# Kernel tuning notes

Hardware: AMD Instinct MI355X
Metric: run time of the kernel (lower is better)

Reference implementation:

```python
import jax, jax.numpy as jnp
import numpy as np

NUM_CODES = 1024
CODE_DIM = 256
BETA = 0.25  # commitment cost
N_TOKENS = 131072


def setup_inputs() -> dict:
    key = jax.random.key(0)
    k_z, k_cb = jax.random.split(key)
    z = jax.random.normal(k_z, (N_TOKENS, CODE_DIM), dtype=jnp.float32)
    # nn.init.uniform_(codebook.weight, -1/num_codes, 1/num_codes)
    codebook = jax.random.uniform(
        k_cb, (NUM_CODES, CODE_DIM), dtype=jnp.float32,
        minval=-1.0 / NUM_CODES, maxval=1.0 / NUM_CODES)
    return {"z": z, "codebook": codebook}


def reference(z, codebook):
    # Squared-euclidean distances: ||z||^2 + ||c||^2 - 2 z c^T  -> [N, K]
    d = (jnp.sum(z * z, axis=1, keepdims=True)
         + jnp.sum(codebook * codebook, axis=1)
         - 2.0 * jnp.einsum('nd,kd->nk', z, codebook))
    indices = jnp.argmin(d, axis=1)          # [N] int
    z_q = codebook[indices]                   # gather [N, D]

    sg = jax.lax.stop_gradient
    commit_loss = BETA * jnp.mean((sg(z) - z_q) ** 2)
    codebook_loss = jnp.mean((z - sg(z_q)) ** 2)
    loss = commit_loss + codebook_loss

    z_st = z + sg(z_q - z)                    # straight-through
    return z_st, indices, loss
```

## Files before the change

### kernel.cpp

```cpp
#include <hip/hip_runtime.h>

#define N_TOK 131072
#define KC    1024
#define DIM   256
#define GAP_THR 4e-4f
#define NBLK  (N_TOK / 128)

typedef __attribute__((ext_vector_type(8)))  short bf16x8;
typedef __attribute__((ext_vector_type(16))) float f32x16;

__device__ __forceinline__ unsigned short f2bf(float f) {
    unsigned int u = __float_as_uint(f);
    unsigned int r = (u + 0x7fffu + ((u >> 16) & 1u)) >> 16;
    return (unsigned short)r;
}

#define WS_NEED 7352384ull

__global__ void vq_prep_cb(const float* __restrict__ cb, unsigned short* __restrict__ cb16,
                           float* __restrict__ cnorm, float* __restrict__ cbT,
                           unsigned int* __restrict__ fcounts) {
    if (blockIdx.x == 0 && threadIdx.x < 2) fcounts[threadIdx.x] = 0u;
    int code = blockIdx.x * 4 + (threadIdx.x >> 6);
    int lane = threadIdx.x & 63;
    float4 v = ((const float4*)cb)[(size_t)code * 64 + lane];
    ((float4*)cbT)[(size_t)lane * KC + code] = v;
    ushort4 h;
    h.x = f2bf(v.x); h.y = f2bf(v.y); h.z = f2bf(v.z); h.w = f2bf(v.w);
    ((ushort4*)cb16)[(size_t)code * 64 + lane] = h;
    double s = 0.0;
    s = fma((double)v.x, (double)v.x, s);
    s = fma((double)v.y, (double)v.y, s);
    s = fma((double)v.z, (double)v.z, s);
    s = fma((double)v.w, (double)v.w, s);
    #pragma unroll
    for (int off = 32; off > 0; off >>= 1) s += __shfl_xor(s, off);
    if (lane == 0) cnorm[code] = (float)s;
}

__global__ __launch_bounds__(256)
void vq_scores_fused(const float* __restrict__ z, const unsigned short* __restrict__ cb16,
                     const float* __restrict__ cb, const float* __restrict__ cnorm,
                     float* __restrict__ out, float* __restrict__ out_idx,
                     int* __restrict__ flist, unsigned int* __restrict__ fcount,
                     double* __restrict__ lparts)
{
    __shared__ uint4  cA[128 * 32];
    __shared__ float  cnsL[KC];
    __shared__ float  bm1L[8][128];
    __shared__ float  gm1[128], gm2[128];
    __shared__ int    gid[128];
    __shared__ double sredD[4];

    const int tid = threadIdx.x;
    const int lane = tid & 63;
    const int l31 = lane & 31;
    const int hi  = lane >> 5;
    const int wid = tid >> 6;
    const int wcode = wid >> 1;
    const int wtok  = wid & 1;
    const int tb = blockIdx.x;

    #pragma unroll
    for (int k = 0; k < 4; ++k) cnsL[tid + k * 256] = cnorm[tid + k * 256];
    if (tid < 128) { gm1[tid] = 3.0e38f; gm2[tid] = 3.0e38f; gid[tid] = 0x7fffffff; }

    bf16x8 bfr[2][4][4];
    float zzr[2];
    #pragma unroll
    for (int f = 0; f < 2; ++f) {
        const int t = tb * 128 + wtok * 64 + f * 32 + l31;
        const float* zr = z + (size_t)t * DIM;
        double s = 0.0;
        #pragma unroll
        for (int kb = 0; kb < 4; ++kb)
            #pragma unroll
            for (int ks = 0; ks < 4; ++ks) {
                const int d0 = kb * 64 + ks * 16 + hi * 8;
                float4 x = *(const float4*)(zr + d0);
                float4 y = *(const float4*)(zr + d0 + 4);
                s = fma((double)x.x, (double)x.x, s);
                s = fma((double)x.y, (double)x.y, s);
                s = fma((double)x.z, (double)x.z, s);
                s = fma((double)x.w, (double)x.w, s);
                s = fma((double)y.x, (double)y.x, s);
                s = fma((double)y.y, (double)y.y, s);
                s = fma((double)y.z, (double)y.z, s);
                s = fma((double)y.w, (double)y.w, s);
                bf16x8 v;
                v[0] = (short)f2bf(x.x); v[1] = (short)f2bf(x.y);
                v[2] = (short)f2bf(x.z); v[3] = (short)f2bf(x.w);
                v[4] = (short)f2bf(y.x); v[5] = (short)f2bf(y.y);
                v[6] = (short)f2bf(y.z); v[7] = (short)f2bf(y.w);
                bfr[f][kb][ks] = v;
            }
        s += __shfl_xor(s, 32);
        zzr[f] = (float)s;
    }

    #pragma unroll 1
    for (int cbk = 0; cbk < 8; ++cbk) {
        __syncthreads();
        #pragma unroll
        for (int i = 0; i < 16; ++i) {
            int g = tid + i * 256;
            int c = g >> 5, u = g & 31;
            cA[c * 32 + (u ^ (c & 7))] = ((const uint4*)cb16)[(size_t)(cbk * 128 + c) * 32 + u];
        }
        __syncthreads();

        f32x16 acc[2][2];
        #pragma unroll
        for (int a = 0; a < 2; ++a)
            #pragma unroll
            for (int b = 0; b < 2; ++b)
                #pragma unroll
                for (int r = 0; r < 16; ++r) acc[a][b][r] = 0.0f;

        #pragma unroll
        for (int kb = 0; kb < 4; ++kb)
            #pragma unroll
            for (int ks = 0; ks < 4; ++ks) {
                bf16x8 af[2];
                #pragma unroll
                for (int a = 0; a < 2; ++a) {
                    int c = wcode * 64 + a * 32 + l31;
                    af[a] = ((const bf16x8*)cA)[c * 32 + ((kb * 8 + ks * 2 + hi) ^ (c & 7))];
                }
                #pragma unroll
                for (int a = 0; a < 2; ++a)
                    #pragma unroll
                    for (int b = 0; b < 2; ++b)
                        acc[a][b] = __builtin_amdgcn_mfma_f32_32x32x16_bf16(af[a], bfr[b][kb][ks], acc[a][b], 0, 0, 0);
            }

        float* sm1 = (float*)cA;
        float* sm2 = sm1 + 256;
        int*   sid = (int*)(sm2 + 256);
        #pragma unroll
        for (int tf = 0; tf < 2; ++tf) {
            float c1 = 3.0e38f, c2 = 3.0e38f;
            #pragma unroll
            for (int cf = 0; cf < 2; ++cf)
                #pragma unroll
                for (int r = 0; r < 16; ++r) {
                    int cl = wcode * 64 + cf * 32 + (r & 3) + 8 * (r >> 2) + 4 * hi;
                    float A  = zzr[tf] + cnsL[cbk * 128 + cl];
                    float dq = fmaf(acc[cf][tf][r], -2.0f, A);
                    acc[cf][tf][r] = dq;
                    float hv = fmaxf(c1, dq);
                    c1 = fminf(c1, dq);
                    c2 = fminf(c2, hv);
                }
            int ci = 0x7fffffff;
            #pragma unroll
            for (int cf = 0; cf < 2; ++cf)
                #pragma unroll
                for (int r = 0; r < 16; ++r) {
                    int code = cbk * 128 + wcode * 64 + cf * 32 + (r & 3) + 8 * (r >> 2) + 4 * hi;
                    ci = min(ci, (acc[cf][tf][r] == c1) ? code : 0x7fffffff);
                }
            float o1 = __shfl_xor(c1, 32);
            float o2 = __shfl_xor(c2, 32);
            int  oi = __shfl_xor(ci, 32);
            float nm2 = fminf(fminf(c2, o2), fmaxf(c1, o1));
            int  ni = (o1 < c1 || (o1 == c1 && oi < ci)) ? oi : ci;
            float nm1 = fminf(c1, o1);
            if (hi == 0) {
                int lt = wtok * 64 + tf * 32 + l31;
                sm1[wcode * 128 + lt] = nm1;
                sm2[wcode * 128 + lt] = nm2;
                sid[wcode * 128 + lt] = ni;
            }
        }
        __syncthreads();
        if (tid < 128) {
            float a1 = sm1[tid],       a2 = sm2[tid];       int ai = sid[tid];
            float b1 = sm1[128 + tid], b2 = sm2[128 + tid]; int bi = sid[128 + tid];
            float m1, m2; int ix;
            if (b1 < a1 || (b1 == a1 && bi < ai)) { m1 = b1; ix = bi; m2 = fminf(b2, a1); }
            else                                   { m1 = a1; ix = ai; m2 = fminf(a2, b1); }
            bm1L[cbk][tid] = m1;
            float g1 = gm1[tid], g2 = gm2[tid]; int gi = gid[tid];
            float ng2 = fminf(fminf(g2, m2), fmaxf(g1, m1));
            if (m1 < g1 || (m1 == g1 && ix < gi)) { g1 = m1; gi = ix; }
            gm1[tid] = g1; gm2[tid] = ng2; gid[tid] = gi;
        }
    }
    __syncthreads();

    if (tid < 128) {
        int row = tb * 128 + tid;
        out_idx[row] = (float)gid[tid];
        float g1 = gm1[tid];
        float gap = gm2[tid] - g1;
        int mask = 0;
        #pragma unroll
        for (int c = 0; c < 8; ++c) mask |= (bm1L[c][tid] <= g1 + GAP_THR) ? (1 << c) : 0;
        if (!(gap > GAP_THR)) {
            unsigned int p = atomicAdd(fcount, 1u);
            flist[p] = row | (mask << 17);
        }
    }
    __syncthreads();

    double ls = 0.0;
    const float4* z4  = (const float4*)z;
    const float4* cb4 = (const float4*)cb;
    float4* out4 = (float4*)out;
    #pragma unroll 4
    for (int it = 0; it < 32; ++it) {
        int fi = tid + it * 256;
        int row = fi >> 6, c4 = fi & 63;
        float4 zv = z4[(size_t)(tb * 128 + row) * 64 + c4];
        int idx = gid[row];
        float4 cv = cb4[(size_t)idx * 64 + c4];
        float4 o;
        o.x = zv.x + (cv.x - zv.x);
        o.y = zv.y + (cv.y - zv.y);
        o.z = zv.z + (cv.z - zv.z);
        o.w = zv.w + (cv.w - zv.w);
        out4[(size_t)(tb * 128 + row) * 64 + c4] = o;
        float dx = zv.x - cv.x, dy = zv.y - cv.y, dz = zv.z - cv.z, dw = zv.w - cv.w;
        ls += (double)dx * dx + (double)dy * dy + (double)dz * dz + (double)dw * dw;
    }
    #pragma unroll
    for (int off = 32; off > 0; off >>= 1) ls += __shfl_down(ls, off);
    if (lane == 0) sredD[wid] = ls;
    __syncthreads();
    if (tid == 0) lparts[tb] = (sredD[0] + sredD[1]) + (sredD[2] + sredD[3]);
}

__global__ void vq_expand(const int* __restrict__ flist, const unsigned int* __restrict__ fcount,
                          int* __restrict__ flist2, unsigned int* __restrict__ fcount2,
                          unsigned long long* __restrict__ rck)
{
    const unsigned int cnt = *fcount;
    for (unsigned int i = blockIdx.x * 256 + threadIdx.x; i < cnt; i += gridDim.x * 256) {
        int e = flist[i];
        int row  = e & 0x1FFFF;
        int mask = ((unsigned int)e) >> 17;
        rck[row] = ~0ull;
        while (mask) {
            int c = __ffs(mask) - 1;
            mask &= mask - 1;
            unsigned int p = atomicAdd(fcount2, 1u);
            flist2[p] = row | (c << 17);
        }
    }
}

__global__ __launch_bounds__(256)
void vq_recheck_pairs(const float* __restrict__ z, const float* __restrict__ cbT,
                      const float* __restrict__ cnorm, const int* __restrict__ flist2,
                      const unsigned int* __restrict__ fcount2,
                      unsigned long long* __restrict__ rck)
{
    const int tid  = threadIdx.x;
    const int wid  = tid >> 6;
    const int lane = tid & 63;
    const unsigned int cnt = *fcount2;

    for (unsigned int p = blockIdx.x * 4 + wid; p < cnt; p += gridDim.x * 4) {
        const int e   = flist2[p];
        const int row = e & 0x1FFFF;
        const int blk = ((unsigned int)e) >> 17;
        const float* zr = z + (size_t)row * DIM;

        float4 zv = ((const float4*)zr)[lane];
        double s = 0.0;
        s = fma((double)zv.x, (double)zv.x, s);
        s = fma((double)zv.y, (double)zv.y, s);
        s = fma((double)zv.z, (double)zv.z, s);
        s = fma((double)zv.w, (double)zv.w, s);
        #pragma unroll
        for (int off = 32; off > 0; off >>= 1) s += __shfl_xor(s, off);
        const float zz = (float)s;

        const int c0 = blk * 128 + lane;
        float e0 = 0.0f, e1 = 0.0f;
        #pragma unroll 8
        for (int d4 = 0; d4 < 64; ++d4) {
            float4 zq = ((const float4*)zr)[d4];
            float4 a  = ((const float4*)cbT)[d4 * KC + c0];
            float4 b  = ((const float4*)cbT)[d4 * KC + c0 + 64];
            e0 = fmaf(zq.x, a.x, e0); e0 = fmaf(zq.y, a.y, e0);
            e0 = fmaf(zq.z, a.z, e0); e0 = fmaf(zq.w, a.w, e0);
            e1 = fmaf(zq.x, b.x, e1); e1 = fmaf(zq.y, b.y, e1);
            e1 = fmaf(zq.z, b.z, e1); e1 = fmaf(zq.w, b.w, e1);
        }
        const float dq0 = fmaf(e0, -2.0f, zz + cnorm[c0]);
        const float dq1 = fmaf(e1, -2.0f, zz + cnorm[c0 + 64]);
        unsigned long long k0 = ((unsigned long long)__float_as_uint(dq0) << 32) | (unsigned int)c0;
        unsigned long long k1 = ((unsigned long long)__float_as_uint(dq1) << 32) | (unsigned int)(c0 + 64);
        unsigned long long k = k0 < k1 ? k0 : k1;
        #pragma unroll
        for (int off = 32; off > 0; off >>= 1) {
            unsigned long long o = __shfl_xor(k, off);
            k = o < k ? o : k;
        }
        if (lane == 0) atomicMin(&rck[row], k);
    }
}

__global__ __launch_bounds__(256)
void vq_fixup(const float* __restrict__ z, const float* __restrict__ cb,
              const int* __restrict__ flist2, const unsigned int* __restrict__ fcount2,
              const unsigned long long* __restrict__ rck,
              float* __restrict__ out, float* __restrict__ out_idx)
{
    const int tid  = threadIdx.x;
    const int wid  = tid >> 6;
    const int lane = tid & 63;
    const unsigned int cnt = *fcount2;

    for (unsigned int p = blockIdx.x * 4 + wid; p < cnt; p += gridDim.x * 4) {
        const int row  = flist2[p] & 0x1FFFF;
        const int code = (int)(unsigned int)rck[row];
        float4 zv = ((const float4*)z)[(size_t)row * 64 + lane];
        float4 cv = ((const float4*)cb)[(size_t)code * 64 + lane];
        float4 o;
        o.x = zv.x + (cv.x - zv.x);
        o.y = zv.y + (cv.y - zv.y);
        o.z = zv.z + (cv.z - zv.z);
        o.w = zv.w + (cv.w - zv.w);
        ((float4*)out)[(size_t)row * 64 + lane] = o;
        if (lane == 0) out_idx[row] = (float)code;
    }
}

__global__ void vq_loss_final(const double* __restrict__ lparts, float* __restrict__ out_loss) {
    __shared__ double s[256];
    const int tid = threadIdx.x;
    double a = 0.0;
    for (int i = tid; i < NBLK; i += 256) a += lparts[i];
    s[tid] = a;
    __syncthreads();
    for (int sft = 128; sft > 0; sft >>= 1) {
        if (tid < sft) s[tid] += s[tid + sft];
        __syncthreads();
    }
    if (tid == 0) {
        float mean = (float)(s[0] / (double)((size_t)N_TOK * DIM));
        out_loss[0] = 0.25f * mean + mean;
    }
}

extern "C" void kernel_launch(void* const* d_in, const int* in_sizes, int n_in,
                              void* d_out, int out_size, void* d_ws, size_t ws_size,
                              hipStream_t stream) {
    const float* z  = (const float*)d_in[0];
    const float* cb = (const float*)d_in[1];
    float* out = (float*)d_out;
    char* ws = (char*)d_ws;

    unsigned short*     cb16    = (unsigned short*)(ws);
    float*              cnorm   = (float*)(ws + 524288);
    float*              cbT     = (float*)(ws + 528384);
    unsigned int*       fcounts = (unsigned int*)(ws + 1576960);
    int*                flist   = (int*)(ws + 1577024);
    int*                flist2  = (int*)(ws + 2101312);
    unsigned long long* rck     = (unsigned long long*)(ws + 6295616);
    double*             lparts  = (double*)(ws + 7344192);

    float* out_idx  = out + (size_t)N_TOK * DIM;
    float* out_loss = out_idx + N_TOK;

    vq_prep_cb<<<KC / 4, 256, 0, stream>>>(cb, cb16, cnorm, cbT, fcounts);
    vq_scores_fused<<<NBLK, 256, 0, stream>>>(z, cb16, cb, cnorm, out, out_idx,
                                              flist, fcounts, lparts);
    vq_expand<<<64, 256, 0, stream>>>(flist, fcounts, flist2, fcounts + 1, rck);
    vq_recheck_pairs<<<2048, 256, 0, stream>>>(z, cbT, cnorm, flist2, fcounts + 1, rck);
    vq_fixup<<<1024, 256, 0, stream>>>(z, cb, flist2, fcounts + 1, rck, out, out_idx);
    vq_loss_final<<<1, 256, 0, stream>>>(lparts, out_loss);
}
```

Before: 326.6 us.

## Fold candidate expansion into scores kernel and track argmin in single pass

Removes the separate vq_expand kernel: the scores kernel now writes per-row/per-chunk recheck pairs and a separate row list for fixup directly, and initialises rck itself. The argmin index is tracked alongside the running min in one pass instead of a second equality scan, and the partial-min scratch gets dedicated shared arrays, so one __syncthreads per chunk can be dropped. The loss accumulation uses a float fma chain before converting to double. This saves a launch and register/ALU work in the epilogue, at the cost of more shared memory, slightly different loss rounding, and more global atomics per ambiguous row.

```diff
diff --git a/kernel.cpp b/kernel.cpp
--- a/kernel.cpp
+++ b/kernel.cpp
@@ -42,14 +42,17 @@
 void vq_scores_fused(const float* __restrict__ z, const unsigned short* __restrict__ cb16,
                      const float* __restrict__ cb, const float* __restrict__ cnorm,
                      float* __restrict__ out, float* __restrict__ out_idx,
-                     int* __restrict__ flist, unsigned int* __restrict__ fcount,
-                     double* __restrict__ lparts)
+                     int* __restrict__ flist2, int* __restrict__ flistR,
+                     unsigned int* __restrict__ fcounts,
+                     unsigned long long* __restrict__ rck, double* __restrict__ lparts)
 {
     __shared__ uint4  cA[128 * 32];
     __shared__ float  cnsL[KC];
     __shared__ float  bm1L[8][128];
     __shared__ float  gm1[128], gm2[128];
     __shared__ int    gid[128];
+    __shared__ float  sm1s[256], sm2s[256];
+    __shared__ int    sids[256];
     __shared__ double sredD[4];
 
     const int tid = threadIdx.x;
@@ -100,7 +103,6 @@
 
     #pragma unroll 1
     for (int cbk = 0; cbk < 8; ++cbk) {
-        __syncthreads();
         #pragma unroll
         for (int i = 0; i < 16; ++i) {
             int g = tid + i * 256;
@@ -134,32 +136,23 @@
                         acc[a][b] = __builtin_amdgcn_mfma_f32_32x32x16_bf16(af[a], bfr[b][kb][ks], acc[a][b], 0, 0, 0);
             }
 
-        float* sm1 = (float*)cA;
-        float* sm2 = sm1 + 256;
-        int*   sid = (int*)(sm2 + 256);
         #pragma unroll
         for (int tf = 0; tf < 2; ++tf) {
             float c1 = 3.0e38f, c2 = 3.0e38f;
+            int rl = 0;
             #pragma unroll
             for (int cf = 0; cf < 2; ++cf)
                 #pragma unroll
                 for (int r = 0; r < 16; ++r) {
-                    int cl = wcode * 64 + cf * 32 + (r & 3) + 8 * (r >> 2) + 4 * hi;
-                    float A  = zzr[tf] + cnsL[cbk * 128 + cl];
+                    int rc = cf * 32 + (r & 3) + 8 * (r >> 2);
+                    float A  = zzr[tf] + cnsL[cbk * 128 + wcode * 64 + rc + 4 * hi];
                     float dq = fmaf(acc[cf][tf][r], -2.0f, A);
-                    acc[cf][tf][r] = dq;
-                    float hv = fmaxf(c1, dq);
-                    c1 = fminf(c1, dq);
-                    c2 = fminf(c2, hv);
+                    bool lt = dq < c1;
+                    c2 = fminf(c2, lt ? c1 : dq);
+                    rl = lt ? rc : rl;
+                    c1 = lt ? dq : c1;
                 }
-            int ci = 0x7fffffff;
-            #pragma unroll
-            for (int cf = 0; cf < 2; ++cf)
-                #pragma unroll
-                for (int r = 0; r < 16; ++r) {
-                    int code = cbk * 128 + wcode * 64 + cf * 32 + (r & 3) + 8 * (r >> 2) + 4 * hi;
-                    ci = min(ci, (acc[cf][tf][r] == c1) ? code : 0x7fffffff);
-                }
+            int ci = cbk * 128 + wcode * 64 + rl + 4 * hi;
             float o1 = __shfl_xor(c1, 32);
             float o2 = __shfl_xor(c2, 32);
             int  oi = __shfl_xor(ci, 32);
@@ -167,16 +160,16 @@
             int  ni = (o1 < c1 || (o1 == c1 && oi < ci)) ? oi : ci;
             float nm1 = fminf(c1, o1);
             if (hi == 0) {
-                int lt = wtok * 64 + tf * 32 + l31;
-                sm1[wcode * 128 + lt] = nm1;
-                sm2[wcode * 128 + lt] = nm2;
-                sid[wcode * 128 + lt] = ni;
+                int lts = wtok * 64 + tf * 32 + l31;
+                sm1s[wcode * 128 + lts] = nm1;
+                sm2s[wcode * 128 + lts] = nm2;
+                sids[wcode * 128 + lts] = ni;
             }
         }
         __syncthreads();
         if (tid < 128) {
-            float a1 = sm1[tid],       a2 = sm2[tid];       int ai = sid[tid];
-            float b1 = sm1[128 + tid], b2 = sm2[128 + tid]; int bi = sid[128 + tid];
+            float a1 = sm1s[tid],       a2 = sm2s[tid];       int ai = sids[tid];
+            float b1 = sm1s[128 + tid], b2 = sm2s[128 + tid]; int bi = sids[128 + tid];
             float m1, m2; int ix;
             if (b1 < a1 || (b1 == a1 && bi < ai)) { m1 = b1; ix = bi; m2 = fminf(b2, a1); }
             else                                   { m1 = a1; ix = ai; m2 = fminf(a2, b1); }
@@ -194,15 +187,18 @@
         out_idx[row] = (float)gid[tid];
         float g1 = gm1[tid];
         float gap = gm2[tid] - g1;
-        int mask = 0;
-        #pragma unroll
-        for (int c = 0; c < 8; ++c) mask |= (bm1L[c][tid] <= g1 + GAP_THR) ? (1 << c) : 0;
         if (!(gap > GAP_THR)) {
-            unsigned int p = atomicAdd(fcount, 1u);
-            flist[p] = row | (mask << 17);
-        }
-    }
-    __syncthreads();
+            rck[row] = ~0ull;
+            unsigned int rp = atomicAdd(fcounts + 1, 1u);
+            flistR[rp] = row;
+            #pragma unroll
+            for (int c = 0; c < 8; ++c)
+                if (bm1L[c][tid] <= g1 + GAP_THR) {
+                    unsigned int p = atomicAdd(fcounts, 1u);
+                    flist2[p] = row | (c << 17);
+                }
+        }
+    }
 
     double ls = 0.0;
     const float4* z4  = (const float4*)z;
@@ -222,7 +218,8 @@
         o.w = zv.w + (cv.w - zv.w);
         out4[(size_t)(tb * 128 + row) * 64 + c4] = o;
         float dx = zv.x - cv.x, dy = zv.y - cv.y, dz = zv.z - cv.z, dw = zv.w - cv.w;
-        ls += (double)dx * dx + (double)dy * dy + (double)dz * dz + (double)dw * dw;
+        float p4 = fmaf(dx, dx, fmaf(dy, dy, fmaf(dz, dz, dw * dw)));
+        ls += (double)p4;
     }
     #pragma unroll
     for (int off = 32; off > 0; off >>= 1) ls += __shfl_down(ls, off);
@@ -231,35 +228,16 @@
     if (tid == 0) lparts[tb] = (sredD[0] + sredD[1]) + (sredD[2] + sredD[3]);
 }
 
-__global__ void vq_expand(const int* __restrict__ flist, const unsigned int* __restrict__ fcount,
-                          int* __restrict__ flist2, unsigned int* __restrict__ fcount2,
-                          unsigned long long* __restrict__ rck)
-{
-    const unsigned int cnt = *fcount;
-    for (unsigned int i = blockIdx.x * 256 + threadIdx.x; i < cnt; i += gridDim.x * 256) {
-        int e = flist[i];
-        int row  = e & 0x1FFFF;
-        int mask = ((unsigned int)e) >> 17;
-        rck[row] = ~0ull;
-        while (mask) {
-            int c = __ffs(mask) - 1;
-            mask &= mask - 1;
-            unsigned int p = atomicAdd(fcount2, 1u);
-            flist2[p] = row | (c << 17);
-        }
-    }
-}
-
 __global__ __launch_bounds__(256)
 void vq_recheck_pairs(const float* __restrict__ z, const float* __restrict__ cbT,
                       const float* __restrict__ cnorm, const int* __restrict__ flist2,
-                      const unsigned int* __restrict__ fcount2,
+                      const unsigned int* __restrict__ fcounts,
                       unsigned long long* __restrict__ rck)
 {
     const int tid  = threadIdx.x;
     const int wid  = tid >> 6;
     const int lane = tid & 63;
-    const unsigned int cnt = *fcount2;
+    const unsigned int cnt = fcounts[0];
 
     for (unsigned int p = blockIdx.x * 4 + wid; p < cnt; p += gridDim.x * 4) {
         const int e   = flist2[p];
@@ -305,17 +283,17 @@
 
 __global__ __launch_bounds__(256)
 void vq_fixup(const float* __restrict__ z, const float* __restrict__ cb,
-              const int* __restrict__ flist2, const unsigned int* __restrict__ fcount2,
+              const int* __restrict__ flistR, const unsigned int* __restrict__ fcounts,
               const unsigned long long* __restrict__ rck,
               float* __restrict__ out, float* __restrict__ out_idx)
 {
     const int tid  = threadIdx.x;
     const int wid  = tid >> 6;
     const int lane = tid & 63;
-    const unsigned int cnt = *fcount2;
+    const unsigned int cnt = fcounts[1];
 
     for (unsigned int p = blockIdx.x * 4 + wid; p < cnt; p += gridDim.x * 4) {
-        const int row  = flist2[p] & 0x1FFFF;
+        const int row  = flistR[p];
         const int code = (int)(unsigned int)rck[row];
         float4 zv = ((const float4*)z)[(size_t)row * 64 + lane];
         float4 cv = ((const float4*)cb)[(size_t)code * 64 + lane];
@@ -358,8 +336,8 @@
     float*              cnorm   = (float*)(ws + 524288);
     float*              cbT     = (float*)(ws + 528384);
     unsigned int*       fcounts = (unsigned int*)(ws + 1576960);
-    int*                flist   = (int*)(ws + 1577024);
-    int*                flist2  = (int*)(ws + 2101312);
+    int*                flist2  = (int*)(ws + 1577024);
+    int*                flistR  = (int*)(ws + 5771328);
     unsigned long long* rck     = (unsigned long long*)(ws + 6295616);
     double*             lparts  = (double*)(ws + 7344192);
 
@@ -368,9 +346,8 @@
 
     vq_prep_cb<<<KC / 4, 256, 0, stream>>>(cb, cb16, cnorm, cbT, fcounts);
     vq_scores_fused<<<NBLK, 256, 0, stream>>>(z, cb16, cb, cnorm, out, out_idx,
-                                              flist, fcounts, lparts);
-    vq_expand<<<64, 256, 0, stream>>>(flist, fcounts, flist2, fcounts + 1, rck);
-    vq_recheck_pairs<<<2048, 256, 0, stream>>>(z, cbT, cnorm, flist2, fcounts + 1, rck);
-    vq_fixup<<<1024, 256, 0, stream>>>(z, cb, flist2, fcounts + 1, rck, out, out_idx);
+                                              flist2, flistR, fcounts, rck, lparts);
+    vq_recheck_pairs<<<2048, 256, 0, stream>>>(z, cbT, cnorm, flist2, fcounts, rck);
+    vq_fixup<<<1024, 256, 0, stream>>>(z, cb, flistR, fcounts, rck, out, out_idx);
     vq_loss_final<<<1, 256, 0, stream>>>(lparts, out_loss);
 }
```

New measurement: 502.6 us. 1.54x slower.
